# Kernel tuning notes

Hardware: AMD Instinct MI355X
Metric: run time of the kernel (lower is better)

Reference implementation:

```python
import jax, jax.numpy as jnp
import numpy as np

N_NODES = 50000


def _graph_conv(x, edges, W0, b0, W1, b1):
    # Symmetric (undirected) message passing: each edge (a,b) sends x[b]->a and x[a]->b.
    src = jnp.concatenate([edges[:, 0], edges[:, 1]])  # [2E]
    dst = jnp.concatenate([edges[:, 1], edges[:, 0]])  # [2E]
    deg = jax.ops.segment_sum(jnp.ones_like(dst, dtype=x.dtype), dst, num_segments=N_NODES)
    deg = jnp.maximum(deg, 1.0)  # avoid div-by-zero for isolated nodes
    agg = jax.ops.segment_sum(x[src], dst, num_segments=N_NODES) / deg[:, None]  # [N, F]
    # self transform + normalized-neighbor transform
    return x @ W0 + b0 + agg @ W1 + b1


def setup_inputs() -> dict:
    key = jax.random.key(0)
    ks = jax.random.split(key, 10)
    feats = [256, 512, 256]  # [in] + hidden + [out]
    inp = {
        "vert_features": jax.random.normal(ks[0], (N_NODES, feats[0]), dtype=jnp.float32),
        "edges": jax.random.randint(ks[1], (400000, 2), 0, N_NODES, dtype=jnp.int64),
    }
    kidx = 2
    for l, (fi, fo) in enumerate(zip(feats[:-1], feats[1:])):
        s = 1.0 / np.sqrt(fi)
        inp[f"W0_{l}"] = jax.random.normal(ks[kidx], (fi, fo), dtype=jnp.float32) * s
        inp[f"b0_{l}"] = jnp.zeros((fo,), dtype=jnp.float32)
        inp[f"W1_{l}"] = jax.random.normal(ks[kidx + 1], (fi, fo), dtype=jnp.float32) * s
        inp[f"b1_{l}"] = jnp.zeros((fo,), dtype=jnp.float32)
        kidx += 2
    return inp


def reference(vert_features, edges, W0_0, b0_0, W1_0, b1_0, W0_1, b0_1, W1_1, b1_1):
    # layer 0 + ReLU
    x = _graph_conv(vert_features, edges, W0_0, b0_0, W1_0, b1_0)
    x = jax.nn.relu(x)
    # final layer (no activation)
    x = _graph_conv(x, edges, W0_1, b0_1, W1_1, b1_1)
    return x
```

## Files before the change

### kernel.cpp

```cpp
#include <hip/hip_runtime.h>
#include <stdint.h>

typedef __bf16  bf16x8 __attribute__((ext_vector_type(8)));
typedef float   f32x4  __attribute__((ext_vector_type(4)));
typedef unsigned short u16x8 __attribute__((ext_vector_type(8)));

__device__ __forceinline__ unsigned short f2bf(float f) {
  unsigned int u = __float_as_uint(f);
  u += 0x7fffu + ((u >> 16) & 1u);
  return (unsigned short)(u >> 16);
}
__device__ __forceinline__ float bflo(unsigned int v) { return __uint_as_float(v << 16); }
__device__ __forceinline__ float bfhi(unsigned int v) { return __uint_as_float(v & 0xffff0000u); }

__device__ __forceinline__ void glds16(const unsigned short* g, unsigned short* l) {
  __builtin_amdgcn_global_load_lds(
      (const __attribute__((address_space(1))) unsigned int*)g,
      (__attribute__((address_space(3))) unsigned int*)l, 16, 0, 0);
}

__device__ __forceinline__ int edges_are_i64(const int* __restrict__ eg) {
  return (eg[1] | eg[3] | eg[5] | eg[7]) == 0;
}

__global__ void phase1_kernel(const float* __restrict__ x, unsigned short* __restrict__ A0, int n,
                              const int* __restrict__ eg, int* __restrict__ deg, int E,
                              const float* __restrict__ W00, const float* __restrict__ W10,
                              const float* __restrict__ W01, const float* __restrict__ W11,
                              const float* __restrict__ b00, const float* __restrict__ b10,
                              const float* __restrict__ b01, const float* __restrict__ b11,
                              unsigned short* __restrict__ Bt1, unsigned short* __restrict__ Bt2,
                              float* __restrict__ bias1, float* __restrict__ bias2) {
  const int i = blockIdx.x * 256 + threadIdx.x;
  if (i < n * 64) {
    const int row = i >> 6, c4 = i & 63;
    const float4 v = ((const float4*)x)[i];
    ushort4 o;
    o.x = f2bf(v.x); o.y = f2bf(v.y); o.z = f2bf(v.z); o.w = f2bf(v.w);
    *(ushort4*)&A0[(size_t)row * 512 + c4 * 4] = o;
  }
  if (i < 512 * 512) {
    const int nn = i >> 9, k = i & 511;
    const float v1 = (k < 256) ? W00[k * 512 + nn] : W10[(k - 256) * 512 + nn];
    Bt1[i] = f2bf(v1);
    const float v2 = (nn < 256) ? W01[k * 256 + nn] : W11[k * 256 + (nn - 256)];
    Bt2[i] = f2bf(v2);
    if (i < 512) {
      bias1[i] = b00[i] + b10[i];
      bias2[i] = (i < 256) ? (b01[i] + b11[i]) : 0.f;
    }
  }
  if (i < E) {
    int a, b;
    if (edges_are_i64(eg)) { a = eg[4 * i]; b = eg[4 * i + 2]; }
    else                   { a = eg[2 * i]; b = eg[2 * i + 1]; }
    if ((unsigned)a < (unsigned)n && (unsigned)b < (unsigned)n) {
      atomicAdd(&deg[a], 1);
      atomicAdd(&deg[b], 1);
    }
  }
}

__global__ void block_sum_kernel(const int* __restrict__ deg, int* __restrict__ bsum, int n) {
  const int t = threadIdx.x;
  const int i = blockIdx.x * 1024 + t;
  int v = (i < n) ? deg[i] : 0;
  #pragma unroll
  for (int d = 32; d > 0; d >>= 1) v += __shfl_xor(v, d);
  __shared__ int ws[16];
  if ((t & 63) == 0) ws[t >> 6] = v;
  __syncthreads();
  if (t < 16) {
    int s = ws[t];
    #pragma unroll
    for (int d = 1; d < 16; d <<= 1) s += __shfl_xor(s, d);
    if (t == 0) bsum[blockIdx.x] = s;
  }
}

__global__ void scan_bsum_kernel(int* __restrict__ bsum, int* __restrict__ off, int nb, int n) {
  const int l = threadIdx.x;
  int v = (l < nb) ? bsum[l] : 0;
  const int orig = v;
  #pragma unroll
  for (int d = 1; d < 64; d <<= 1) {
    int u = __shfl_up(v, d);
    if (l >= d) v += u;
  }
  if (l < nb) bsum[l] = v - orig;
  if (l == nb - 1) off[n] = v;
}

__global__ void scan_final_kernel(const int* __restrict__ deg, const int* __restrict__ bsum,
                                  int* __restrict__ off, float* __restrict__ invd,
                                  int* __restrict__ curp, int n) {
  const int t = threadIdx.x;
  const int i = blockIdx.x * 1024 + t;
  const int lane = t & 63, wid = t >> 6;
  const int v = (i < n) ? deg[i] : 0;
  int s = v;
  #pragma unroll
  for (int d = 1; d < 64; d <<= 1) {
    int u = __shfl_up(s, d);
    if (lane >= d) s += u;
  }
  __shared__ int ws[16];
  if (lane == 63) ws[wid] = s;
  __syncthreads();
  if (t < 16) {
    int w = ws[t];
    #pragma unroll
    for (int d = 1; d < 16; d <<= 1) {
      int u = __shfl_up(w, d);
      if (t >= d) w += u;
    }
    ws[t] = w;
  }
  __syncthreads();
  const int add = (wid > 0) ? ws[wid - 1] : 0;
  const int incl = s + add;
  if (i < n) {
    off[i] = bsum[blockIdx.x] + incl - v;
    invd[i] = 1.f / (float)(v > 1 ? v : 1);
    curp[i] = 0;
  }
}

__global__ void fill_kernel(const int* __restrict__ eg,
                            const int* __restrict__ off, int* __restrict__ cur,
                            int* __restrict__ adj, int E, int n) {
  const int e = blockIdx.x * 256 + threadIdx.x;
  if (e >= E) return;
  int a, b;
  if (edges_are_i64(eg)) { a = eg[4 * e]; b = eg[4 * e + 2]; }
  else                   { a = eg[2 * e]; b = eg[2 * e + 1]; }
  if ((unsigned)a >= (unsigned)n || (unsigned)b >= (unsigned)n) return;
  int p = atomicAdd(&cur[b], 1); adj[off[b] + p] = a;
  int q = atomicAdd(&cur[a], 1); adj[off[a] + q] = b;
}

template<int MODE>
__global__ __launch_bounds__(256) void agg_wide_kernel(
    const unsigned short* __restrict__ T, unsigned short* A0w, float* out,
    const int* __restrict__ adj, const int* __restrict__ off,
    const float* __restrict__ invd, int n) {
  const int node = blockIdx.x * 4 + (threadIdx.x >> 6);
  if (node >= n) return;
  const int lane = threadIdx.x & 63;
  const int half = lane >> 5;
  const int cq = lane & 31;
  constexpr size_t RS = (MODE == 0) ? 512 : 256;
  const int s = off[node], e = off[node + 1];
  float a0 = 0.f, a1 = 0.f, a2 = 0.f, a3 = 0.f, a4 = 0.f, a5 = 0.f, a6 = 0.f, a7 = 0.f;
  for (int base = s; base < e; base += 64) {
    const int cnt = min(64, e - base);
    const int idxv = (lane < cnt) ? adj[base + lane] : 0;
    for (int j = 0; j < cnt; j += 8) {
      uint4 v0 = make_uint4(0u, 0u, 0u, 0u), v1 = v0, v2 = v0, v3 = v0;
      const int s0 = j + 0 + half, s1 = j + 2 + half, s2 = j + 4 + half, s3 = j + 6 + half;
      const int r0 = __shfl(idxv, s0), r1 = __shfl(idxv, s1);
      const int r2 = __shfl(idxv, s2), r3 = __shfl(idxv, s3);
      if (s0 < cnt) v0 = *(const uint4*)&T[(size_t)r0 * RS + cq * 8];
      if (s1 < cnt) v1 = *(const uint4*)&T[(size_t)r1 * RS + cq * 8];
      if (s2 < cnt) v2 = *(const uint4*)&T[(size_t)r2 * RS + cq * 8];
      if (s3 < cnt) v3 = *(const uint4*)&T[(size_t)r3 * RS + cq * 8];
      a0 += bflo(v0.x) + bflo(v1.x) + bflo(v2.x) + bflo(v3.x);
      a1 += bfhi(v0.x) + bfhi(v1.x) + bfhi(v2.x) + bfhi(v3.x);
      a2 += bflo(v0.y) + bflo(v1.y) + bflo(v2.y) + bflo(v3.y);
      a3 += bfhi(v0.y) + bfhi(v1.y) + bfhi(v2.y) + bfhi(v3.y);
      a4 += bflo(v0.z) + bflo(v1.z) + bflo(v2.z) + bflo(v3.z);
      a5 += bfhi(v0.z) + bfhi(v1.z) + bfhi(v2.z) + bfhi(v3.z);
      a6 += bflo(v0.w) + bflo(v1.w) + bflo(v2.w) + bflo(v3.w);
      a7 += bfhi(v0.w) + bfhi(v1.w) + bfhi(v2.w) + bfhi(v3.w);
    }
  }
  a0 += __shfl_xor(a0, 32); a1 += __shfl_xor(a1, 32);
  a2 += __shfl_xor(a2, 32); a3 += __shfl_xor(a3, 32);
  a4 += __shfl_xor(a4, 32); a5 += __shfl_xor(a5, 32);
  a6 += __shfl_xor(a6, 32); a7 += __shfl_xor(a7, 32);
  if (half == 0) {
    const float sc = invd[node];
    if (MODE == 0) {
      u16x8 o;
      o[0] = f2bf(a0 * sc); o[1] = f2bf(a1 * sc); o[2] = f2bf(a2 * sc); o[3] = f2bf(a3 * sc);
      o[4] = f2bf(a4 * sc); o[5] = f2bf(a5 * sc); o[6] = f2bf(a6 * sc); o[7] = f2bf(a7 * sc);
      *(u16x8*)&A0w[(size_t)node * 512 + 256 + cq * 8] = o;
    } else {
      float* po = &out[(size_t)node * 256 + cq * 8];
      float4 p0 = *(float4*)po;
      float4 p1 = *(float4*)(po + 4);
      p0.x += sc * a0; p0.y += sc * a1; p0.z += sc * a2; p0.w += sc * a3;
      p1.x += sc * a4; p1.y += sc * a5; p1.z += sc * a6; p1.w += sc * a7;
      *(float4*)po = p0;
      *(float4*)(po + 4) = p1;
    }
  }
}

__global__ __launch_bounds__(512, 2) void fused_gemm_kernel(
    const unsigned short* __restrict__ A, const unsigned short* __restrict__ B1,
    const unsigned short* __restrict__ B2,
    const float* __restrict__ bias1, const float* __restrict__ bias2,
    float* __restrict__ Pout, unsigned short* __restrict__ Zout, int M_real) {
  __shared__ __attribute__((aligned(16))) char smem[147456];
  unsigned short* sA  = (unsigned short*)smem;
  unsigned short* sB  = (unsigned short*)(smem + 32768);
  unsigned short* Hl  = (unsigned short*)smem;
  unsigned short* sB2 = (unsigned short*)(smem + 131072);
  const int t = threadIdx.x;
  const int lane = t & 63;
  const int wid = t >> 6;
  const int wr = wid >> 2;
  const int wc = wid & 3;
  const int m0 = blockIdx.x * 128;

  f32x4 acc1[2][4][4];
  #pragma unroll
  for (int c = 0; c < 2; ++c)
    #pragma unroll
    for (int m = 0; m < 4; ++m)
      #pragma unroll
      for (int n = 0; n < 4; ++n)
        acc1[c][m][n] = f32x4{0.f, 0.f, 0.f, 0.f};

  #pragma unroll
  for (int nc1 = 0; nc1 < 2; ++nc1) {
    auto stageA = [&](int buf, int kt) {
      #pragma unroll
      for (int i = 0; i < 2; ++i) {
        const int row = (t >> 3) + i * 64;
        const int c = (t & 7) ^ (row & 7);
        glds16(A + (size_t)(m0 + row) * 512 + kt * 64 + c * 8,
               &sA[buf * 8192 + (i * 512 + t) * 8]);
      }
      #pragma unroll
      for (int i = 0; i < 4; ++i) {
        const int row = (t >> 3) + i * 64;
        const int c = (t & 7) ^ (row & 7);
        glds16(B1 + (size_t)(nc1 * 256 + row) * 512 + kt * 64 + c * 8,
               &sB[buf * 16384 + (i * 512 + t) * 8]);
      }
    };
    stageA(0, 0);
    __syncthreads();
    #pragma unroll 1
    for (int kt = 0; kt < 8; ++kt) {
      if (kt < 7) stageA((kt + 1) & 1, kt + 1);
      const int buf = kt & 1;
      #pragma unroll
      for (int kk = 0; kk < 2; ++kk) {
        bf16x8 aF[4], bF[4];
        #pragma unroll
        for (int m = 0; m < 4; ++m) {
          const int row = wr * 64 + m * 16 + (lane & 15);
          const int sl = (kk * 4 + (lane >> 4)) ^ (row & 7);
          aF[m] = *(const bf16x8*)&sA[buf * 8192 + row * 64 + sl * 8];
        }
        #pragma unroll
        for (int n = 0; n < 4; ++n) {
          const int rl = wc * 64 + n * 16 + (lane & 15);
          const int sl = (kk * 4 + (lane >> 4)) ^ (rl & 7);
          bF[n] = *(const bf16x8*)&sB[buf * 16384 + rl * 64 + sl * 8];
        }
        #pragma unroll
        for (int m = 0; m < 4; ++m)
          #pragma unroll
          for (int n = 0; n < 4; ++n)
            acc1[nc1][m][n] = __builtin_amdgcn_mfma_f32_16x16x32_bf16(aF[m], bF[n], acc1[nc1][m][n], 0, 0, 0);
      }
      __syncthreads();
    }
  }

  #pragma unroll
  for (int nc1 = 0; nc1 < 2; ++nc1) {
    #pragma unroll
    for (int n = 0; n < 4; ++n) {
      const int col = nc1 * 256 + wc * 64 + n * 16 + (lane & 15);
      const float bc = bias1[col];
      #pragma unroll
      for (int m = 0; m < 4; ++m) {
        #pragma unroll
        for (int r = 0; r < 4; ++r) {
          const int row = wr * 64 + m * 16 + (lane >> 4) * 4 + r;
          float y = acc1[nc1][m][n][r] + bc;
          y = y > 0.f ? y : 0.f;
          Hl[row * 512 + (((col >> 3) ^ (row & 7)) << 3) + (col & 7)] = f2bf(y);
        }
      }
    }
  }
  __syncthreads();

  #pragma unroll 1
  for (int g = 0; g < 4; ++g) {
    f32x4 acc2[4][2];
    #pragma unroll
    for (int m = 0; m < 4; ++m)
      #pragma unroll
      for (int n = 0; n < 2; ++n)
        acc2[m][n] = f32x4{0.f, 0.f, 0.f, 0.f};

    auto stageB2 = [&](int buf, int kt) {
      const int row = t >> 2;
      const int c = (t & 3) ^ ((row >> 1) & 3);
      glds16(B2 + (size_t)(g * 128 + row) * 512 + kt * 32 + c * 8,
             &sB2[buf * 4096 + t * 8]);
    };
    stageB2(0, 0);
    __syncthreads();
    #pragma unroll 1
    for (int kt = 0; kt < 16; ++kt) {
      if (kt < 15) stageB2((kt + 1) & 1, kt + 1);
      const int buf = kt & 1;
      bf16x8 aF2[4], bF2[2];
      #pragma unroll
      for (int m = 0; m < 4; ++m) {
        const int hr = wr * 64 + m * 16 + (lane & 15);
        const int chk = (kt * 4 + (lane >> 4)) ^ (hr & 7);
        aF2[m] = *(const bf16x8*)&Hl[hr * 512 + chk * 8];
      }
      #pragma unroll
      for (int n = 0; n < 2; ++n) {
        const int rl = wc * 32 + n * 16 + (lane & 15);
        const int sl = (lane >> 4) ^ ((rl >> 1) & 3);
        bF2[n] = *(const bf16x8*)&sB2[buf * 4096 + rl * 32 + sl * 8];
      }
      #pragma unroll
      for (int m = 0; m < 4; ++m)
        #pragma unroll
        for (int n = 0; n < 2; ++n)
          acc2[m][n] = __builtin_amdgcn_mfma_f32_16x16x32_bf16(aF2[m], bF2[n], acc2[m][n], 0, 0, 0);
      __syncthreads();
    }

    if (g < 2) {
      #pragma unroll
      for (int n = 0; n < 2; ++n) {
        const int gcol = g * 128 + wc * 32 + n * 16 + (lane & 15);
        const float bc = bias2[gcol];
        #pragma unroll
        for (int m = 0; m < 4; ++m) {
          #pragma unroll
          for (int r = 0; r < 4; ++r) {
            const int grow = m0 + wr * 64 + m * 16 + (lane >> 4) * 4 + r;
            if (grow < M_real) Pout[(size_t)grow * 256 + gcol] = acc2[m][n][r] + bc;
          }
        }
      }
    } else {
      unsigned short* rep = sB2;
      #pragma unroll
      for (int h = 0; h < 2; ++h) {
        if (wr == h) {
          #pragma unroll
          for (int n = 0; n < 2; ++n) {
            const int lcol = wc * 32 + n * 16 + (lane & 15);
            #pragma unroll
            for (int m = 0; m < 4; ++m)
              #pragma unroll
              for (int r = 0; r < 4; ++r) {
                const int lr = m * 16 + (lane >> 4) * 4 + r;
                rep[lr * 128 + (lcol ^ (((lr >> 2) & 7) << 4))] = f2bf(acc2[m][n][r]);
              }
          }
        }
        __syncthreads();
        #pragma unroll
        for (int p = 0; p < 2; ++p) {
          const int idx = p * 512 + t;
          const int tr = idx >> 4;
          const int cb = (idx & 15) * 8;
          const uint4 v = *(const uint4*)&rep[tr * 128 + (cb ^ (((tr >> 2) & 7) << 4))];
          *(uint4*)&Zout[(size_t)(m0 + h * 64 + tr) * 256 + (g - 2) * 128 + cb] = v;
        }
        __syncthreads();
      }
    }
  }
}

extern "C" void kernel_launch(void* const* d_in, const int* in_sizes, int n_in,
                              void* d_out, int out_size, void* d_ws, size_t ws_size,
                              hipStream_t stream) {
  const float* x   = (const float*)d_in[0];
  const int* edges = (const int*)d_in[1];
  const float* W00 = (const float*)d_in[2];
  const float* b00 = (const float*)d_in[3];
  const float* W10 = (const float*)d_in[4];
  const float* b10 = (const float*)d_in[5];
  const float* W01 = (const float*)d_in[6];
  const float* b01 = (const float*)d_in[7];
  const float* W11 = (const float*)d_in[8];
  const float* b11 = (const float*)d_in[9];
  float* out = (float*)d_out;

  const int n = in_sizes[0] / 256;
  const int E = in_sizes[1] / 2;
  const int Mpad = ((n + 127) / 128) * 128;
  const int nstrip = (n + 127) / 128;
  const int Mp = nstrip * 128;

  char* p = (char*)d_ws;
  auto alloc = [&](size_t bytes) { char* r = p; p += (bytes + 255) & ~(size_t)255; return r; };
  unsigned short* A0   = (unsigned short*)alloc((size_t)Mp * 512 * 2);
  unsigned short* Z    = (unsigned short*)alloc((size_t)Mp * 256 * 2);
  unsigned short* Bt1  = (unsigned short*)alloc(512 * 512 * 2);
  unsigned short* Bt2  = (unsigned short*)alloc(512 * 512 * 2);
  float* bias1 = (float*)alloc(512 * 4);
  float* bias2 = (float*)alloc(512 * 4);
  int*   deg   = (int*)alloc((size_t)n * 4);
  int*   curp  = (int*)alloc((size_t)n * 4);
  int*   off   = (int*)alloc((size_t)(n + 1) * 4);
  int*   bsum  = (int*)alloc(256 * 4);
  float* invd  = (float*)alloc((size_t)n * 4);
  int*   adj   = (int*)alloc((size_t)2 * E * 4);

  hipMemsetAsync(deg, 0, (size_t)n * 4, stream);

  const int p1_blocks = (n * 64 + 255) / 256;
  phase1_kernel<<<p1_blocks, 256, 0, stream>>>(x, A0, n, edges, deg, E,
                                               W00, W10, W01, W11, b00, b10, b01, b11,
                                               Bt1, Bt2, bias1, bias2);

  const int nb = (n + 1023) / 1024;
  block_sum_kernel<<<nb, 1024, 0, stream>>>(deg, bsum, n);
  scan_bsum_kernel<<<1, 64, 0, stream>>>(bsum, off, nb, n);
  scan_final_kernel<<<nb, 1024, 0, stream>>>(deg, bsum, off, invd, curp, n);
  fill_kernel<<<(E + 255) / 256, 256, 0, stream>>>(edges, off, curp, adj, E, n);

  agg_wide_kernel<0><<<(n + 3) / 4, 256, 0, stream>>>(A0, A0, nullptr, adj, off, invd, n);

  fused_gemm_kernel<<<nstrip, 512, 0, stream>>>(A0, Bt1, Bt2, bias1, bias2, out, Z, n);

  agg_wide_kernel<1><<<(n + 3) / 4, 256, 0, stream>>>(Z, nullptr, out, adj, off, invd, n);
}
```

Measured before the change: 329.6 us.

## Compute all four output groups of second GEMM in one K loop

The second GEMM in the fused kernel used to loop over four 128-column output groups, re-reading the hidden tile from LDS for each group. It now keeps accumulators for all 512 columns at once and stages the full 512-row B2 slice per K step, so each A fragment is loaded once and reused across all groups. LDS grows to 160KB and the per-K-step double buffering is dropped in favour of a synchronous load with two barriers. Accumulator registers quadruple, which risks spills or lower occupancy under the 512x2 launch bounds, and there is no longer any overlap between B2 loads and MFMA work.

```diff
diff --git a/kernel.cpp b/kernel.cpp
--- a/kernel.cpp
+++ b/kernel.cpp
@@ -202,7 +202,7 @@
     const unsigned short* __restrict__ B2,
     const float* __restrict__ bias1, const float* __restrict__ bias2,
     float* __restrict__ Pout, unsigned short* __restrict__ Zout, int M_real) {
-  __shared__ __attribute__((aligned(16))) char smem[147456];
+  __shared__ __attribute__((aligned(16))) char smem[163840];
   unsigned short* sA  = (unsigned short*)smem;
   unsigned short* sB  = (unsigned short*)(smem + 32768);
   unsigned short* Hl  = (unsigned short*)smem;
@@ -292,91 +292,93 @@
   }
   __syncthreads();
 
+  f32x4 acc2[4][4][2];
+  #pragma unroll
+  for (int g = 0; g < 4; ++g)
+    #pragma unroll
+    for (int m = 0; m < 4; ++m)
+      #pragma unroll
+      for (int n = 0; n < 2; ++n)
+        acc2[g][m][n] = f32x4{0.f, 0.f, 0.f, 0.f};
+
   #pragma unroll 1
-  for (int g = 0; g < 4; ++g) {
-    f32x4 acc2[4][2];
-    #pragma unroll
-    for (int m = 0; m < 4; ++m)
-      #pragma unroll
-      for (int n = 0; n < 2; ++n)
-        acc2[m][n] = f32x4{0.f, 0.f, 0.f, 0.f};
-
-    auto stageB2 = [&](int buf, int kt) {
-      const int row = t >> 2;
-      const int c = (t & 3) ^ ((row >> 1) & 3);
-      glds16(B2 + (size_t)(g * 128 + row) * 512 + kt * 32 + c * 8,
-             &sB2[buf * 4096 + t * 8]);
-    };
-    stageB2(0, 0);
+  for (int kt = 0; kt < 16; ++kt) {
     __syncthreads();
-    #pragma unroll 1
-    for (int kt = 0; kt < 16; ++kt) {
-      if (kt < 15) stageB2((kt + 1) & 1, kt + 1);
-      const int buf = kt & 1;
-      bf16x8 aF2[4], bF2[2];
+    #pragma unroll
+    for (int i = 0; i < 4; ++i) {
+      const int idx = i * 512 + t;
+      const int row = idx >> 2;
+      const int c = (idx & 3) ^ ((row >> 1) & 3);
+      glds16(B2 + (size_t)row * 512 + kt * 32 + c * 8, &sB2[idx * 8]);
+    }
+    __syncthreads();
+    bf16x8 aF2[4];
+    #pragma unroll
+    for (int m = 0; m < 4; ++m) {
+      const int hr = wr * 64 + m * 16 + (lane & 15);
+      const int chk = (kt * 4 + (lane >> 4)) ^ (hr & 7);
+      aF2[m] = *(const bf16x8*)&Hl[hr * 512 + chk * 8];
+    }
+    #pragma unroll
+    for (int g = 0; g < 4; ++g) {
+      bf16x8 bF2[2];
+      #pragma unroll
+      for (int n = 0; n < 2; ++n) {
+        const int rl = g * 128 + wc * 32 + n * 16 + (lane & 15);
+        const int sl = (lane >> 4) ^ ((rl >> 1) & 3);
+        bF2[n] = *(const bf16x8*)&sB2[rl * 32 + sl * 8];
+      }
+      #pragma unroll
+      for (int m = 0; m < 4; ++m)
+        #pragma unroll
+        for (int n = 0; n < 2; ++n)
+          acc2[g][m][n] = __builtin_amdgcn_mfma_f32_16x16x32_bf16(aF2[m], bF2[n], acc2[g][m][n], 0, 0, 0);
+    }
+  }
+  __syncthreads();
+
+  #pragma unroll
+  for (int g = 0; g < 2; ++g) {
+    #pragma unroll
+    for (int n = 0; n < 2; ++n) {
+      const int gcol = g * 128 + wc * 32 + n * 16 + (lane & 15);
+      const float bc = bias2[gcol];
       #pragma unroll
       for (int m = 0; m < 4; ++m) {
-        const int hr = wr * 64 + m * 16 + (lane & 15);
-        const int chk = (kt * 4 + (lane >> 4)) ^ (hr & 7);
-        aF2[m] = *(const bf16x8*)&Hl[hr * 512 + chk * 8];
-      }
-      #pragma unroll
-      for (int n = 0; n < 2; ++n) {
-        const int rl = wc * 32 + n * 16 + (lane & 15);
-        const int sl = (lane >> 4) ^ ((rl >> 1) & 3);
-        bF2[n] = *(const bf16x8*)&sB2[buf * 4096 + rl * 32 + sl * 8];
-      }
-      #pragma unroll
-      for (int m = 0; m < 4; ++m)
-        #pragma unroll
-        for (int n = 0; n < 2; ++n)
-          acc2[m][n] = __builtin_amdgcn_mfma_f32_16x16x32_bf16(aF2[m], bF2[n], acc2[m][n], 0, 0, 0);
-      __syncthreads();
-    }
-
-    if (g < 2) {
-      #pragma unroll
-      for (int n = 0; n < 2; ++n) {
-        const int gcol = g * 128 + wc * 32 + n * 16 + (lane & 15);
-        const float bc = bias2[gcol];
-        #pragma unroll
-        for (int m = 0; m < 4; ++m) {
-          #pragma unroll
-          for (int r = 0; r < 4; ++r) {
-            const int grow = m0 + wr * 64 + m * 16 + (lane >> 4) * 4 + r;
-            if (grow < M_real) Pout[(size_t)grow * 256 + gcol] = acc2[m][n][r] + bc;
-          }
+        #pragma unroll
+        for (int r = 0; r < 4; ++r) {
+          const int grow = m0 + wr * 64 + m * 16 + (lane >> 4) * 4 + r;
+          if (grow < M_real) Pout[(size_t)grow * 256 + gcol] = acc2[g][m][n][r] + bc;
         }
       }
-    } else {
-      unsigned short* rep = sB2;
-      #pragma unroll
-      for (int h = 0; h < 2; ++h) {
-        if (wr == h) {
-          #pragma unroll
-          for (int n = 0; n < 2; ++n) {
-            const int lcol = wc * 32 + n * 16 + (lane & 15);
-            #pragma unroll
-            for (int m = 0; m < 4; ++m)
-              #pragma unroll
-              for (int r = 0; r < 4; ++r) {
-                const int lr = m * 16 + (lane >> 4) * 4 + r;
-                rep[lr * 128 + (lcol ^ (((lr >> 2) & 7) << 4))] = f2bf(acc2[m][n][r]);
-              }
-          }
+    }
+  }
+
+  #pragma unroll 1
+  for (int g = 2; g < 4; ++g) {
+    unsigned short* rep = sB2;
+    #pragma unroll
+    for (int n = 0; n < 2; ++n) {
+      const int lcol = wc * 32 + n * 16 + (lane & 15);
+      #pragma unroll
+      for (int m = 0; m < 4; ++m) {
+        #pragma unroll
+        for (int r = 0; r < 4; ++r) {
+          const int lr = wr * 64 + m * 16 + (lane >> 4) * 4 + r;
+          rep[lr * 128 + (lcol ^ (((lr >> 2) & 7) << 4))] = f2bf(acc2[g][m][n][r]);
         }
-        __syncthreads();
-        #pragma unroll
-        for (int p = 0; p < 2; ++p) {
-          const int idx = p * 512 + t;
-          const int tr = idx >> 4;
-          const int cb = (idx & 15) * 8;
-          const uint4 v = *(const uint4*)&rep[tr * 128 + (cb ^ (((tr >> 2) & 7) << 4))];
-          *(uint4*)&Zout[(size_t)(m0 + h * 64 + tr) * 256 + (g - 2) * 128 + cb] = v;
-        }
-        __syncthreads();
-      }
-    }
+      }
+    }
+    __syncthreads();
+    #pragma unroll
+    for (int p = 0; p < 4; ++p) {
+      const int idx = p * 512 + t;
+      const int tr = idx >> 4;
+      const int cb = (idx & 15) * 8;
+      const uint4 v = *(const uint4*)&rep[tr * 128 + (cb ^ (((tr >> 2) & 7) << 4))];
+      *(uint4*)&Zout[(size_t)(m0 + tr) * 256 + (g - 2) * 128 + cb] = v;
+    }
+    __syncthreads();
   }
 }
 
@@ -397,7 +399,6 @@
 
   const int n = in_sizes[0] / 256;
   const int E = in_sizes[1] / 2;
-  const int Mpad = ((n + 127) / 128) * 128;
   const int nstrip = (n + 127) / 128;
   const int Mp = nstrip * 128;
 
```

Measured after the change: 588.6 us. +78.6%, slower.
